# Kernel optimization log

Measured on AMD Instinct MI355X. Metric: run time of the kernel, lower is better.

## Reference

```python
import jax, jax.numpy as jnp
import numpy as np

B, L = 8, 128            # batch, max_length
VF = 32128               # full (padded) T5 vocab in logits
V = 32100                # act_vocab_size (codebook entries)
D = 768                  # embed_dim
TAU = 1.0                # gumbel-softmax temperature
EPS = 1e-8               # cosine-similarity eps (torch default)


def setup_inputs() -> dict:
    key = jax.random.key(0)
    k1, k2, k3, k4, k5 = jax.random.split(key, 5)
    logits = jax.random.normal(k1, (B, L, VF), jnp.float32)
    u = jax.random.uniform(k2, (B, L, VF), jnp.float32, 1e-6, 1.0 - 1e-6)
    gumbel_noise = -jnp.log(-jnp.log(u))
    word_embeddings = jax.random.normal(k3, (V, D), jnp.float32) * 0.02
    # rewrite attention mask: ones prefix of random length per row
    lengths = jax.random.randint(k4, (B,), 1, L)
    rwrt_attention = (jnp.arange(L)[None, :] < lengths[:, None]).astype(jnp.int32)
    psg_input = jax.random.randint(k5, (B, L), 0, V)
    # mimic torch.roll(psg_input, 1, 1); psg_input[:, 0] = 1
    psg_input = jnp.roll(psg_input, 1, axis=1).at[:, 0].set(1)
    return dict(logits=logits, gumbel_noise=gumbel_noise,
                word_embeddings=word_embeddings,
                rwrt_attention=rwrt_attention, psg_input=psg_input)


def reference(logits, gumbel_noise, word_embeddings, rwrt_attention, psg_input):
    # --- hard gumbel-softmax (straight-through) ---
    y = jax.nn.softmax((logits + gumbel_noise) / TAU, axis=-1)      # [B,L,VF]
    hard = jax.nn.one_hot(jnp.argmax(y, axis=-1), VF, dtype=y.dtype)
    g = hard + y - jax.lax.stop_gradient(y)
    g = g[..., :V]                                                   # [B,L,V]

    # --- soft codebook lookup (one-hot @ embedding table) ---
    embeds = jnp.einsum('blv,vd->bld', g, word_embeddings)           # [B,L,D]
    embeds = embeds * rwrt_attention.astype(embeds.dtype)[:, :, None]

    # --- passage extraction + per-row roll-by-gather ---
    flipped = jnp.fliplr(rwrt_attention)
    keep = 1 - flipped
    extr = (keep.astype(psg_input.dtype)) * psg_input                # [B,L]
    shifts = jnp.sum(rwrt_attention == 1, axis=1)                    # [B]
    pos = jnp.arange(L)
    src = (pos[None, :] - shifts[:, None]) % L                       # right-roll
    idx = jnp.take_along_axis(extr, src, axis=1)                     # [B,L]

    # flag-gated embedding lookup: skip leading zeros, then always gather
    flag = jnp.cumsum((idx != 0).astype(jnp.int32), axis=1) > 0      # [B,L]
    psg_emb = jnp.where(flag[:, :, None], word_embeddings[idx], 0.0)
    embeds = embeds + psg_emb                                        # [B,L,D]

    # --- brute-force cosine-similarity NN decode over the codebook ---
    rn = embeds / jnp.maximum(jnp.linalg.norm(embeds, axis=-1, keepdims=True), EPS)
    wn = word_embeddings / jnp.maximum(
        jnp.linalg.norm(word_embeddings, axis=-1, keepdims=True), EPS)
    sims = jnp.einsum('bld,vd->blv', rn, wn)                         # [B,L,V]
    nn_idx = jnp.argmax(sims, axis=-1)                               # [B,L]
    return embeds, nn_idx
```

## Files before the change

### kernel.cpp

```cpp
#include <hip/hip_runtime.h>
#include <math.h>
#include <limits.h>

#define B_  8
#define L_  128
#define VF_ 32128
#define V_  32100
#define D_  768

#define SEGS_ 2
#define NV4_  (VF_ / 4)
#define HALF_ (NV4_ / 2)

typedef unsigned long long u64;

__device__ __forceinline__ unsigned int fmap(float f) {
    unsigned int u = __float_as_uint(f);
    return (u & 0x80000000u) ? ~u : (u | 0x80000000u);
}

__global__ __launch_bounds__(256, 8) void k_argmax(
    const float* __restrict__ logits, const float* __restrict__ gumbel,
    u64* __restrict__ keys)
{
    const int row  = blockIdx.x >> 1;
    const int half = blockIdx.x & 1;
    const int tid  = threadIdx.x;
    const size_t rowoff = (size_t)row * VF_;
    const float4* lp = (const float4*)(logits + rowoff);
    const float4* gp = (const float4*)(gumbel + rowoff);

    float bv = -INFINITY;
    int   bi = 0;
    int   i  = half * HALF_ + tid;
    #pragma unroll 4
    for (int it = 0; it < 16; ++it) {
        const int ii = (i < NV4_ - 1) ? i : (NV4_ - 1);
        const float4 a = lp[ii];
        const float4 g = gp[ii];
        float v;
        v = a.x + g.x; if (v > bv) { bv = v; bi = 4*ii + 0; }
        v = a.y + g.y; if (v > bv) { bv = v; bi = 4*ii + 1; }
        v = a.z + g.z; if (v > bv) { bv = v; bi = 4*ii + 2; }
        v = a.w + g.w; if (v > bv) { bv = v; bi = 4*ii + 3; }
        i += 256;
    }

    u64 k = ((u64)fmap(bv) << 32) | (u64)(VF_ - bi);
    for (int off = 32; off > 0; off >>= 1) {
        u64 o = __shfl_down(k, off, 64);
        if (o > k) k = o;
    }
    __shared__ u64 s_k[4];
    if ((tid & 63) == 0) s_k[tid >> 6] = k;
    __syncthreads();
    if (tid == 0) {
        u64 kk = s_k[0];
        if (s_k[1] > kk) kk = s_k[1];
        if (s_k[2] > kk) kk = s_k[2];
        if (s_k[3] > kk) kk = s_k[3];
        keys[blockIdx.x] = kk;
    }
}

__global__ __launch_bounds__(192) void k_emb(
    const float* __restrict__ W,
    const int* __restrict__ rwrt, const int* __restrict__ psg,
    const u64* __restrict__ keys,
    float* __restrict__ out, float* __restrict__ nn_out)
{
    const int row = blockIdx.x;
    const int b = row >> 7;
    const int l = row & 127;
    const int t = threadIdx.x;

    __shared__ int s_att[L_];
    __shared__ int s_extr[L_];
    __shared__ u64 s_keys[SEGS_];
    __shared__ int s_len, s_first, s_rA, s_rB;

    if (t == 0) s_first = INT_MAX;
    if (t < L_) s_att[t] = rwrt[b * L_ + t];
    if (t >= 128 && t < 128 + SEGS_) s_keys[t - 128] = keys[row * SEGS_ + (t - 128)];
    __syncthreads();

    if (t == 0) {
        int len = 0;
        for (int i = 0; i < L_; ++i) len += (s_att[i] == 1);
        s_len = len;
    }
    if (t < L_) s_extr[t] = (1 - s_att[L_ - 1 - t]) * psg[b * L_ + t];
    __syncthreads();

    if (t < L_) {
        int src = (t - s_len + L_) & (L_ - 1);
        if (s_extr[src] != 0) atomicMin(&s_first, t);
    }
    __syncthreads();

    if (t == 0) {
        u64 kk = s_keys[0];
        #pragma unroll
        for (int i = 1; i < SEGS_; ++i) if (s_keys[i] > kk) kk = s_keys[i];
        const int am   = VF_ - (int)(kk & 0xFFFFFFFFull);
        const int srcl = (l - s_len + L_) & (L_ - 1);
        const int idxv = s_extr[srcl];
        const int flag = (l >= s_first) ? 1 : 0;
        const int rA = (s_att[l] == 1 && am < V_) ? am : -1;
        const int rB = flag ? idxv : -1;
        s_rA = rA; s_rB = rB;
        const int nn = (rA >= 0) ? rA : ((rB >= 0) ? rB : 0);
        nn_out[row] = (float)nn;
    }
    __syncthreads();

    const int rA = s_rA;
    const int rB = s_rB;
    float4 v = make_float4(0.f, 0.f, 0.f, 0.f);
    if (rA >= 0) {
        float4 a = ((const float4*)(W + (size_t)rA * D_))[t];
        v.x += a.x; v.y += a.y; v.z += a.z; v.w += a.w;
    }
    if (rB >= 0) {
        float4 a = ((const float4*)(W + (size_t)rB * D_))[t];
        v.x += a.x; v.y += a.y; v.z += a.z; v.w += a.w;
    }
    ((float4*)(out + (size_t)row * D_))[t] = v;
}

extern "C" void kernel_launch(void* const* d_in, const int* in_sizes, int n_in,
                              void* d_out, int out_size, void* d_ws, size_t ws_size,
                              hipStream_t stream)
{
    const float* logits = (const float*)d_in[0];
    const float* gumbel = (const float*)d_in[1];
    const float* W      = (const float*)d_in[2];
    const int*   rwrt   = (const int*)d_in[3];
    const int*   psg    = (const int*)d_in[4];

    float* out    = (float*)d_out;
    float* nn_out = out + (size_t)B_ * L_ * D_;

    u64* keys = (u64*)d_ws;

    k_argmax<<<B_ * L_ * SEGS_, 256, 0, stream>>>(logits, gumbel, keys);
    k_emb<<<B_ * L_, 192, 0, stream>>>(W, rwrt, psg, keys, out, nn_out);
}
```

Baseline: 321.0 us.

## Stream argmax inputs through LDS with async global_load_lds pipeline

Replaces the direct float4 register loads in the argmax kernel with asynchronous global-to-LDS loads (global_load_lds), kept four stages deep in a ring buffer. Hand-placed vmcnt waits let each wave consume one stage while later loads are in flight. The goal is more memory-level parallelism on a bandwidth-bound streaming reduction. In exchange it uses 32KB of LDS per block and lowers the occupancy hint from 8 to 5, and it relies on inline asm for wait counting.

Measured after the change: 309.0 us. 1.04x faster.

```diff
diff --git a/kernel.cpp b/kernel.cpp
--- a/kernel.cpp
+++ b/kernel.cpp
@@ -13,46 +13,92 @@
 #define HALF_ (NV4_ / 2)
 
 typedef unsigned long long u64;
+typedef float f4 __attribute__((ext_vector_type(4)));
+typedef const __attribute__((address_space(1))) void* as1p;
+typedef __attribute__((address_space(3))) void* as3p;
 
 __device__ __forceinline__ unsigned int fmap(float f) {
     unsigned int u = __float_as_uint(f);
     return (u & 0x80000000u) ? ~u : (u | 0x80000000u);
 }
 
-__global__ __launch_bounds__(256, 8) void k_argmax(
+__global__ __launch_bounds__(256, 5) void k_argmax(
     const float* __restrict__ logits, const float* __restrict__ gumbel,
     u64* __restrict__ keys)
 {
+    __shared__ char lds_raw[32768];
+
     const int row  = blockIdx.x >> 1;
     const int half = blockIdx.x & 1;
     const int tid  = threadIdx.x;
+    const int w    = tid >> 6;
+    const int lane = tid & 63;
     const size_t rowoff = (size_t)row * VF_;
-    const float4* lp = (const float4*)(logits + rowoff);
-    const float4* gp = (const float4*)(gumbel + rowoff);
+    const float* lpf = logits + rowoff;
+    const float* gpf = gumbel + rowoff;
+    const int cbase = half * HALF_ + w * 64;
+    const unsigned woff  = (unsigned)(w * 1024);
+    const unsigned lbase = (unsigned)(size_t)(__attribute__((address_space(3))) char*)lds_raw;
+
+#define ISSUE(j) do {                                                         \
+    const int i_ = cbase + (j)*256 + lane;                                    \
+    const int ii_ = (i_ < NV4_-1) ? i_ : (NV4_-1);                            \
+    const unsigned so_ = (unsigned)(((j)&3)*8192) + woff;                     \
+    __builtin_amdgcn_global_load_lds((as1p)(lpf + (size_t)ii_*4),             \
+                                     (as3p)(lds_raw + so_),        16, 0, 0); \
+    __builtin_amdgcn_global_load_lds((as1p)(gpf + (size_t)ii_*4),             \
+                                     (as3p)(lds_raw + so_ + 4096), 16, 0, 2); \
+} while (0)
+
+#define CONSUME(it, K) do {                                                   \
+    f4 aL, aG;                                                                \
+    const unsigned off_ = lbase + (unsigned)(((it)&3)*8192) + woff            \
+                        + (unsigned)(lane*16);                                \
+    asm volatile("s_waitcnt vmcnt(" #K ")\n\t"                                \
+                 "ds_read_b128 %0, %2\n\t"                                    \
+                 "ds_read_b128 %1, %2 offset:4096\n\t"                        \
+                 "s_waitcnt lgkmcnt(0)"                                       \
+                 : "=v"(aL), "=v"(aG) : "v"(off_) : "memory");                \
+    const int i_ = cbase + (it)*256 + lane;                                   \
+    const int ii_ = (i_ < NV4_-1) ? i_ : (NV4_-1);                            \
+    float v_;                                                                 \
+    v_ = aL[0]+aG[0]; if (v_>bv){bv=v_; bi=4*ii_+0;}                          \
+    v_ = aL[1]+aG[1]; if (v_>bv){bv=v_; bi=4*ii_+1;}                          \
+    v_ = aL[2]+aG[2]; if (v_>bv){bv=v_; bi=4*ii_+2;}                          \
+    v_ = aL[3]+aG[3]; if (v_>bv){bv=v_; bi=4*ii_+3;}                          \
+} while (0)
 
     float bv = -INFINITY;
     int   bi = 0;
-    int   i  = half * HALF_ + tid;
-    #pragma unroll 4
-    for (int it = 0; it < 16; ++it) {
-        const int ii = (i < NV4_ - 1) ? i : (NV4_ - 1);
-        const float4 a = lp[ii];
-        const float4 g = gp[ii];
-        float v;
-        v = a.x + g.x; if (v > bv) { bv = v; bi = 4*ii + 0; }
-        v = a.y + g.y; if (v > bv) { bv = v; bi = 4*ii + 1; }
-        v = a.z + g.z; if (v > bv) { bv = v; bi = 4*ii + 2; }
-        v = a.w + g.w; if (v > bv) { bv = v; bi = 4*ii + 3; }
-        i += 256;
-    }
+
+    ISSUE(0); ISSUE(1); ISSUE(2); ISSUE(3);
+    CONSUME(0, 6);  ISSUE(4);
+    CONSUME(1, 6);  ISSUE(5);
+    CONSUME(2, 6);  ISSUE(6);
+    CONSUME(3, 6);  ISSUE(7);
+    CONSUME(4, 6);  ISSUE(8);
+    CONSUME(5, 6);  ISSUE(9);
+    CONSUME(6, 6);  ISSUE(10);
+    CONSUME(7, 6);  ISSUE(11);
+    CONSUME(8, 6);  ISSUE(12);
+    CONSUME(9, 6);  ISSUE(13);
+    CONSUME(10, 6); ISSUE(14);
+    CONSUME(11, 6); ISSUE(15);
+    CONSUME(12, 6);
+    CONSUME(13, 4);
+    CONSUME(14, 2);
+    CONSUME(15, 0);
+#undef ISSUE
+#undef CONSUME
 
     u64 k = ((u64)fmap(bv) << 32) | (u64)(VF_ - bi);
     for (int off = 32; off > 0; off >>= 1) {
         u64 o = __shfl_down(k, off, 64);
         if (o > k) k = o;
     }
-    __shared__ u64 s_k[4];
-    if ((tid & 63) == 0) s_k[tid >> 6] = k;
+    __syncthreads();
+    u64* s_k = (u64*)lds_raw;
+    if (lane == 0) s_k[w] = k;
     __syncthreads();
     if (tid == 0) {
         u64 kk = s_k[0];
```
